# Kernel optimization log

Measured on AMD Instinct MI355X. Metric: run time of the kernel, lower is better.

The kernel has to match this reference:

```python
import jax, jax.numpy as jnp
import numpy as np

B, S, D, H, L, V, F = 4, 2048, 512, 8, 4, 32000, 512
EPS = 1e-3  # keras BatchNormalization default epsilon


def setup_inputs() -> dict:
    key = jax.random.key(0)
    ks = jax.random.split(key, 32)
    n = lambda k, shp, sc=0.02: (jax.random.normal(k, shp, jnp.float32) * sc)
    inp = {
        "sequence": jax.random.randint(ks[0], (B, S), 0, V, dtype=jnp.int32),
        # padding mask: 1 for kept tokens, 0 for padded; broadcast over [B,h,S,S]
        "padding_mask": (jax.random.uniform(ks[1], (B, 1, 1, S)) > 0.1).astype(jnp.float32),
        "pos_embeddings": n(ks[2], (S, D), 1.0),
        "emb": n(ks[3], (V, D), 1.0),
        "wq": n(ks[4], (L, D, D)), "bq": jnp.zeros((L, D), jnp.float32),
        "wk": n(ks[5], (L, D, D)), "bk": jnp.zeros((L, D), jnp.float32),
        "wv": n(ks[6], (L, D, D)), "bv": jnp.zeros((L, D), jnp.float32),
        "wo": n(ks[7], (L, D, D)), "bo": jnp.zeros((L, D), jnp.float32),
        "an_gamma": 1.0 + n(ks[8], (L, D)), "an_beta": n(ks[9], (L, D)),
        "an_mean": n(ks[10], (L, D), 0.1), "an_var": 0.5 + jax.random.uniform(ks[11], (L, D)),
        "d1_w": n(ks[12], (L, D, F)), "d1_b": jnp.zeros((L, F), jnp.float32),
        "d2_w": n(ks[13], (L, F, D)), "d2_b": jnp.zeros((L, D), jnp.float32),
        "fn_gamma": 1.0 + n(ks[14], (L, D)), "fn_beta": n(ks[15], (L, D)),
        "fn_mean": n(ks[16], (L, D), 0.1), "fn_var": 0.5 + jax.random.uniform(ks[17], (L, D)),
    }
    return inp


def _bn(x, gamma, beta, mean, var):
    # keras BatchNormalization in inference mode (moving statistics), axis=-1
    return (x - mean) * jax.lax.rsqrt(var + EPS) * gamma + beta


def reference(sequence, padding_mask, pos_embeddings, emb,
              wq, bq, wk, bk, wv, bv, wo, bo,
              an_gamma, an_beta, an_mean, an_var,
              d1_w, d1_b, d2_w, d2_b,
              fn_gamma, fn_beta, fn_mean, fn_var):
    b, s = sequence.shape
    nlayers, d, _ = wq.shape
    h = H
    dk = d // h
    scale = 1.0 / jnp.sqrt(jnp.float32(dk))

    x = emb[sequence] + pos_embeddings[:s, :]  # [B,S,D]

    def split_heads(t):  # [B,S,D] -> [B,h,S,dk]
        return t.reshape(b, s, h, dk).transpose(0, 2, 1, 3)

    for i in range(nlayers):
        q = split_heads(x @ wq[i] + bq[i])
        k = split_heads(x @ wk[i] + bk[i])
        v = split_heads(x @ wv[i] + bv[i])
        score = jnp.einsum('bhqd,bhkd->bhqk', q, k) * scale  # [B,h,S,S]
        if padding_mask is not None:
            score = score * padding_mask
            score = jnp.where(score == 0, jnp.float32(-1e9), score)
        align = jax.nn.softmax(score, axis=-1)
        ctx = jnp.einsum('bhqk,bhkd->bhqd', align, v)
        ctx = ctx.transpose(0, 2, 1, 3).reshape(b, s, d)
        heads = ctx @ wo[i] + bo[i]
        sub = _bn(x + heads, an_gamma[i], an_beta[i], an_mean[i], an_var[i])
        ffn = jax.nn.relu(sub @ d1_w[i] + d1_b[i]) @ d2_w[i] + d2_b[i]
        x = _bn(sub + ffn, fn_gamma[i], fn_beta[i], fn_mean[i], fn_var[i])
    return x
```

## Files before the change

kernel.cpp:

```cpp
#include <hip/hip_runtime.h>
#include <stdint.h>
#include <stddef.h>

constexpr int BB = 4, SS = 2048, DD = 512, HH = 8, LL = 4;
constexpr int NTOK = BB * SS;
constexpr float BN_EPS = 1e-3f;

using bh = __bf16;
typedef __bf16 bf16x8 __attribute__((ext_vector_type(8)));
typedef float  f32x4  __attribute__((ext_vector_type(4)));

#define DEV __device__ __forceinline__
#define WAITVM(n) asm volatile("s_waitcnt vmcnt(" #n ")" ::: "memory")
#define WAITLGKM0 asm volatile("s_waitcnt lgkmcnt(0)" ::: "memory")

DEV void gload_lds16(const void* g, void* l) {
    __builtin_amdgcn_global_load_lds(
        (const __attribute__((address_space(1))) void*)g,
        (__attribute__((address_space(3))) void*)l, 16, 0, 0);
}

__global__ void wprep(const float* __restrict__ in, bh* __restrict__ out, int ostride) {
    __shared__ float t[32][33];
    const float* ip = in + (size_t)blockIdx.z * DD * DD;
    bh* op = out + (size_t)blockIdx.z * ostride;
    const int r0 = blockIdx.y * 32, c0 = blockIdx.x * 32;
    const int tx = threadIdx.x, ty = threadIdx.y;
    #pragma unroll
    for (int i = ty; i < 32; i += 8) t[i][tx] = ip[(size_t)(r0 + i) * DD + c0 + tx];
    __syncthreads();
    #pragma unroll
    for (int i = ty; i < 32; i += 8) op[(size_t)(c0 + i) * DD + r0 + tx] = (bh)t[tx][i];
}

__global__ void maskprep(const float* __restrict__ mask, float* __restrict__ mb) {
    const int i = ((int)blockIdx.x * 256 + threadIdx.x) * 4;
    const float4 m4 = *(const float4*)(mask + i);
    float4 o;
    o.x = (m4.x == 0.f) ? -1e30f : 0.f;
    o.y = (m4.y == 0.f) ? -1e30f : 0.f;
    o.z = (m4.z == 0.f) ? -1e30f : 0.f;
    o.w = (m4.w == 0.f) ? -1e30f : 0.f;
    *(float4*)(mb + i) = o;
}

__global__ void embed_k(const int* __restrict__ seq, const float* __restrict__ emb,
                        const float* __restrict__ pos, bh* __restrict__ xb) {
    const int m = blockIdx.x;
    const int s = m & (SS - 1);
    const int tok = seq[m];
    const int d = threadIdx.x * 4;
    const float4 e  = *(const float4*)(emb + (size_t)tok * DD + d);
    const float4 pz = *(const float4*)(pos + (size_t)s * DD + d);
    union { bh h[4]; uint64_t u; } pk;
    pk.h[0] = (bh)(e.x + pz.x); pk.h[1] = (bh)(e.y + pz.y);
    pk.h[2] = (bh)(e.z + pz.z); pk.h[3] = (bh)(e.w + pz.w);
    *(uint64_t*)(xb + (size_t)m * DD + d) = pk.u;
}


template <int EP, bool WF32>
__global__ __launch_bounds__(256, 2)
void gemm_bt(const bh* __restrict__ A, const bh* __restrict__ Bt,
             const float* __restrict__ bias, bh* __restrict__ outb,
             const bh* __restrict__ resb, float* __restrict__ Xo,
             const float* __restrict__ gamma, const float* __restrict__ beta,
             const float* __restrict__ mean, const float* __restrict__ var) {
    constexpr int BM = 128, BN = 64, BK = 64, NKT = DD / BK;
    __shared__ __align__(16) bh As[2][BM * BK];
    __shared__ __align__(16) bh Bs[2][BN * BK];

    const int tid = threadIdx.x;
    const int w = tid >> 6, lane = tid & 63;
    const int l15 = lane & 15, l4 = lane >> 4;
    const int i = (int)blockIdx.x;
    const int xcd = i & 7, j = i >> 3;
    const int bm = xcd * 8 + (j >> 3);
    const int bn = j & 7;
    const int m0 = bm * BM, n0 = bn * BN;
    const int wr = w >> 1, wc = w & 1;

    f32x4 acc[4][2] = {};
    const int sr = lane >> 3;
    const int cbx = (lane & 7) ^ sr;

    auto stage = [&](int buf, int kk) {
        #pragma unroll
        for (int ii = 0; ii < 4; ++ii) {
            const int idx = w * 4 + ii;
            const int r = idx * 8 + sr;
            gload_lds16(A + (size_t)(m0 + r) * DD + kk + 8 * cbx, &As[buf][idx * 512]);
        }
        #pragma unroll
        for (int ii = 0; ii < 2; ++ii) {
            const int idx = w * 2 + ii;
            const int r = idx * 8 + sr;
            gload_lds16(Bt + (size_t)(n0 + r) * DD + kk + 8 * cbx, &Bs[buf][idx * 512]);
        }
    };

    stage(0, 0);
    stage(1, BK);

    for (int kt = 0; kt < NKT; ++kt) {
        const int buf = kt & 1;
        if (kt + 1 < NKT) { WAITVM(6); } else { WAITVM(0); }
        __builtin_amdgcn_s_barrier();

        const char* Ab = (const char*)&As[buf][0];
        const char* Bb = (const char*)&Bs[buf][0];
        #pragma unroll
        for (int ks = 0; ks < 2; ++ks) {
            bf16x8 af[4], bfr[2];
            const int cby = ks * 64 + l4 * 16;
            #pragma unroll
            for (int mf = 0; mf < 4; ++mf) {
                const int row = wr * 64 + mf * 16 + l15;
                af[mf] = *(const bf16x8*)(Ab + row * 128 + (cby ^ ((row & 7) << 4)));
            }
            #pragma unroll
            for (int nf = 0; nf < 2; ++nf) {
                const int row = wc * 32 + nf * 16 + l15;
                bfr[nf] = *(const bf16x8*)(Bb + row * 128 + (cby ^ ((row & 7) << 4)));
            }
            #pragma unroll
            for (int mf = 0; mf < 4; ++mf)
                #pragma unroll
                for (int nf = 0; nf < 2; ++nf)
                    acc[mf][nf] = __builtin_amdgcn_mfma_f32_16x16x32_bf16(
                        af[mf], bfr[nf], acc[mf][nf], 0, 0, 0);
        }
        WAITLGKM0;
        __builtin_amdgcn_s_barrier();
        if (kt + 2 < NKT) stage(buf, (kt + 2) * BK);
    }

    #pragma unroll
    for (int nf = 0; nf < 2; ++nf) {
        const int n = n0 + wc * 32 + nf * 16 + l15;
        const float bi = bias[n];
        float g = 0.f, be = 0.f, mu = 0.f, iv = 0.f;
        if constexpr (EP == 1) {
            g = gamma[n]; be = beta[n]; mu = mean[n];
            iv = rsqrtf(var[n] + BN_EPS);
        }
        #pragma unroll
        for (int mf = 0; mf < 4; ++mf) {
            #pragma unroll
            for (int r = 0; r < 4; ++r) {
                const int m = m0 + wr * 64 + mf * 16 + l4 * 4 + r;
                const size_t off = (size_t)m * DD + n;
                const float v = acc[mf][nf][r] + bi;
                if constexpr (EP == 2) {
                    outb[off] = (bh)fmaxf(v, 0.f);
                } else {
                    const float t = (float)resb[off] + v;
                    const float s = (t - mu) * iv * g + be;
                    outb[off] = (bh)s;
                    if constexpr (WF32) Xo[off] = s;
                }
            }
        }
    }
}

__global__ __launch_bounds__(256, 3)
void gemm_qkv(const bh* __restrict__ A, const bh* __restrict__ Bt,
              const float* __restrict__ bq, const float* __restrict__ bk,
              const float* __restrict__ bv,
              bh* __restrict__ qb, bh* __restrict__ kb, bh* __restrict__ vT) {
    constexpr int BM = 128, BN = 64, BK = 64, NKT = DD / BK;
    __shared__ __align__(16) bh As[2][BM * BK];
    __shared__ __align__(16) bh Bs[2][BN * BK];

    const int tid = threadIdx.x;
    const int w = tid >> 6, lane = tid & 63;
    const int l15 = lane & 15, l4 = lane >> 4;
    const int i = (int)blockIdx.x;
    const int xcd = i & 7, j = i >> 3;
    const int bm = xcd * 8 + (j & 7);
    const int bn = j >> 3;
    const int m0 = bm * BM, n0 = bn * BN;
    const int wr = w >> 1, wc = w & 1;

    f32x4 acc[4][2] = {};
    const int sr = lane >> 3;
    const int cbx = (lane & 7) ^ sr;

    auto stage = [&](int buf, int kk) {
        #pragma unroll
        for (int ii = 0; ii < 4; ++ii) {
            const int idx = w * 4 + ii;
            const int r = idx * 8 + sr;
            gload_lds16(A + (size_t)(m0 + r) * DD + kk + 8 * cbx, &As[buf][idx * 512]);
        }
        #pragma unroll
        for (int ii = 0; ii < 2; ++ii) {
            const int idx = w * 2 + ii;
            const int r = idx * 8 + sr;
            gload_lds16(Bt + (size_t)(n0 + r) * DD + kk + 8 * cbx, &Bs[buf][idx * 512]);
        }
    };

    stage(0, 0);
    stage(1, BK);

    for (int kt = 0; kt < NKT; ++kt) {
        const int buf = kt & 1;
        if (kt + 1 < NKT) { WAITVM(6); } else { WAITVM(0); }
        __builtin_amdgcn_s_barrier();

        const char* Ab = (const char*)&As[buf][0];
        const char* Bb = (const char*)&Bs[buf][0];
        #pragma unroll
        for (int ks = 0; ks < 2; ++ks) {
            bf16x8 af[4], bfr[2];
            const int cby = ks * 64 + l4 * 16;
            #pragma unroll
            for (int mf = 0; mf < 4; ++mf) {
                const int row = wr * 64 + mf * 16 + l15;
                af[mf] = *(const bf16x8*)(Ab + row * 128 + (cby ^ ((row & 7) << 4)));
            }
            #pragma unroll
            for (int nf = 0; nf < 2; ++nf) {
                const int row = wc * 32 + nf * 16 + l15;
                bfr[nf] = *(const bf16x8*)(Bb + row * 128 + (cby ^ ((row & 7) << 4)));
            }
            #pragma unroll
            for (int mf = 0; mf < 4; ++mf)
                #pragma unroll
                for (int nf = 0; nf < 2; ++nf)
                    acc[mf][nf] = __builtin_amdgcn_mfma_f32_16x16x32_bf16(
                        af[mf], bfr[nf], acc[mf][nf], 0, 0, 0);
        }
        WAITLGKM0;
        __builtin_amdgcn_s_barrier();
        if (kt + 2 < NKT) stage(buf, (kt + 2) * BK);
    }

    const int part = n0 >> 9;
    #pragma unroll
    for (int nf = 0; nf < 2; ++nf) {
        const int n = n0 + wc * 32 + nf * 16 + l15;
        const int nn = n & 511;
        const float bi = (part == 0 ? bq : part == 1 ? bk : bv)[nn];
        if (part < 2) {
            bh* out = part ? kb : qb;
            #pragma unroll
            for (int mf = 0; mf < 4; ++mf)
                #pragma unroll
                for (int r = 0; r < 4; ++r) {
                    const int m = m0 + wr * 64 + mf * 16 + l4 * 4 + r;
                    out[(size_t)m * DD + nn] = (bh)(acc[mf][nf][r] + bi);
                }
        } else {
            const int hh = nn >> 6, dk = nn & 63;
            #pragma unroll
            for (int mf = 0; mf < 4; ++mf) {
                const int m = m0 + wr * 64 + mf * 16 + l4 * 4;
                const int bb2 = m >> 11, s = m & (SS - 1);
                union { bh h4[4]; uint64_t u; } pk;
                #pragma unroll
                for (int r = 0; r < 4; ++r)
                    pk.h4[r] = (bh)(acc[mf][nf][r] + bi);
                *(uint64_t*)(vT + ((size_t)((bb2 * HH + hh) * 64) + dk) * SS + s) = pk.u;
            }
        }
    }
}

__global__ __launch_bounds__(128, 2)
void flash_attn(const bh* __restrict__ Q, const bh* __restrict__ K,
                const bh* __restrict__ VT, const float* __restrict__ mb,
                bh* __restrict__ O) {
    constexpr int KVB = 64, NT = SS / KVB;
    constexpr float CSC = 0.18033688f;
    __shared__ __align__(16) bh Ks[2][KVB * 64];
    __shared__ __align__(16) bh Vs[2][64 * KVB];
    __shared__ __align__(16) bh Plds[2][2][16 * 64];

    const int tid = threadIdx.x;
    const int w = tid >> 6, lane = tid & 63;
    const int l15 = lane & 15, l4 = lane >> 4;

    const int i = (int)blockIdx.x;
    const int xcd = i & 7, j = i >> 3;
    const int g = xcd * 4 + (j >> 5);
    const int qt = j & 31;
    const int h = g & 7, b = g >> 3;

    const int q0 = qt * 64 + w * 32;

    bf16x8 qf[2][2];
    #pragma unroll
    for (int st = 0; st < 2; ++st) {
        const bh* qp = Q + (size_t)(b * SS + q0 + st * 16 + l15) * DD + h * 64 + l4 * 8;
        qf[st][0] = *(const bf16x8*)qp;
        qf[st][1] = *(const bf16x8*)(qp + 32);
    }

    f32x4 ctx[2][4] = {};
    f32x4 accl[2] = {};
    float m2[2] = {-3e38f, -3e38f};

    bf16x8 ones;
    #pragma unroll
    for (int z = 0; z < 8; ++z) ones[z] = (bh)1.0f;

    const int sr = lane >> 3;
    const int cbx = (lane & 7) ^ sr;
    const bh* kg = K + (size_t)b * SS * DD + h * 64 + 8 * cbx;
    const bh* vg = VT + (size_t)((b * HH + h) * 64) * SS + 8 * cbx;
    const float* mbb = mb + (size_t)b * SS;

    auto stage = [&](int buf, int kt) {
        #pragma unroll
        for (int ii = 0; ii < 4; ++ii) {
            const int idx = w * 4 + ii;
            const int r = idx * 8 + sr;
            gload_lds16(kg + (size_t)(kt + r) * DD, &Ks[buf][idx * 512]);
        }
        #pragma unroll
        for (int ii = 0; ii < 4; ++ii) {
            const int idx = w * 4 + ii;
            const int r = idx * 8 + sr;
            gload_lds16(vg + (size_t)r * SS + kt, &Vs[buf][idx * 512]);
        }
    };

    f32x4 mbc[4];
    stage(0, 0);
    stage(1, KVB);
    #pragma unroll
    for (int nf = 0; nf < 4; ++nf)
        mbc[nf] = *(const f32x4*)(mbb + nf * 16 + l4 * 4);
    __syncthreads();

    for (int t = 0; t < NT; ++t) {
        const int buf = t & 1;
        const int kt = t * KVB;
        if (t > 0) {
            if (t + 1 < NT) { WAITVM(12); } else { WAITVM(4); }
            __builtin_amdgcn_s_barrier();
        }

        f32x4 sc[2][4] = {};
        const char* Kb = (const char*)&Ks[buf][0];
        #pragma unroll
        for (int ks = 0; ks < 2; ++ks) {
            bf16x8 kf[4];
            #pragma unroll
            for (int nf = 0; nf < 4; ++nf) {
                const int row = nf * 16 + l15;
                kf[nf] = *(const bf16x8*)(Kb + row * 128 +
                          ((ks * 64 + l4 * 16) ^ ((row & 7) << 4)));
            }
            __builtin_amdgcn_s_setprio(1);
            #pragma unroll
            for (int st = 0; st < 2; ++st)
                #pragma unroll
                for (int nf = 0; nf < 4; ++nf)
                    sc[st][nf] = __builtin_amdgcn_mfma_f32_16x16x32_bf16(
                        kf[nf], qf[st][ks], sc[st][nf], 0, 0, 0);
            __builtin_amdgcn_s_setprio(0);
        }

        #pragma unroll
        for (int st = 0; st < 2; ++st) {
            #pragma unroll
            for (int nf = 0; nf < 4; ++nf)
                #pragma unroll
                for (int r = 0; r < 4; ++r)
                    sc[st][nf][r] = fmaf(sc[st][nf][r], CSC, mbc[nf][r]);
            float tm;
            {
                f32x4 m01, m23;
                #pragma unroll
                for (int r = 0; r < 4; ++r) {
                    m01[r] = fmaxf(sc[st][0][r], sc[st][1][r]);
                    m23[r] = fmaxf(sc[st][2][r], sc[st][3][r]);
                }
                const float a = fmaxf(fmaxf(m01[0], m01[1]), fmaxf(m01[2], m01[3]));
                const float c = fmaxf(fmaxf(m23[0], m23[1]), fmaxf(m23[2], m23[3]));
                tm = fmaxf(a, c);
            }
            tm = fmaxf(tm, __shfl_xor(tm, 16, 64));
            tm = fmaxf(tm, __shfl_xor(tm, 32, 64));
            if (__any(tm > m2[st] + 11.5f)) {
                const float mn = fmaxf(fmaxf(tm, m2[st]), -60.f);
                const float fac = __builtin_amdgcn_exp2f(m2[st] - mn);
                m2[st] = mn;
                accl[st] *= fac;
                #pragma unroll
                for (int nf = 0; nf < 4; ++nf)
                    #pragma unroll
                    for (int r = 0; r < 4; ++r)
                        ctx[st][nf][r] *= fac;
            }
            #pragma unroll
            for (int nf = 0; nf < 4; ++nf) {
                union { bh h4[4]; uint64_t u; } pk;
                #pragma unroll
                for (int r = 0; r < 4; ++r)
                    pk.h4[r] = (bh)__builtin_amdgcn_exp2f(sc[st][nf][r] - m2[st]);
                *(uint64_t*)((char*)&Plds[w][st][0] + l15 * 128 +
                             ((nf * 32 + l4 * 8) ^ ((l15 & 7) << 4))) = pk.u;
            }
        }

        const char* Vb = (const char*)&Vs[buf][0];
        #pragma unroll
        for (int ks = 0; ks < 2; ++ks) {
            bf16x8 vf[4];
            #pragma unroll
            for (int nf = 0; nf < 4; ++nf) {
                const int row = nf * 16 + l15;
                vf[nf] = *(const bf16x8*)(Vb + row * 128 +
                          ((ks * 64 + l4 * 16) ^ ((row & 7) << 4)));
            }
            bf16x8 pa[2];
            #pragma unroll
            for (int st = 0; st < 2; ++st)
                pa[st] = *(const bf16x8*)((const char*)&Plds[w][st][0] + l15 * 128 +
                          ((ks * 64 + l4 * 16) ^ ((l15 & 7) << 4)));
            __builtin_amdgcn_s_setprio(1);
            #pragma unroll
            for (int st = 0; st < 2; ++st) {
                #pragma unroll
                for (int nf = 0; nf < 4; ++nf)
                    ctx[st][nf] = __builtin_amdgcn_mfma_f32_16x16x32_bf16(
                        vf[nf], pa[st], ctx[st][nf], 0, 0, 0);
                accl[st] = __builtin_amdgcn_mfma_f32_16x16x32_bf16(
                    ones, pa[st], accl[st], 0, 0, 0);
            }
            __builtin_amdgcn_s_setprio(0);
        }

        WAITLGKM0;
        __builtin_amdgcn_s_barrier();
        if (t + 1 < NT) {
            #pragma unroll
            for (int nf = 0; nf < 4; ++nf)
                mbc[nf] = *(const f32x4*)(mbb + kt + KVB + nf * 16 + l4 * 4);
        }
        if (t + 2 < NT) stage(buf, kt + 2 * KVB);
    }

    #pragma unroll
    for (int st = 0; st < 2; ++st) {
        const float linv = 1.0f / accl[st][0];
        #pragma unroll
        for (int nf = 0; nf < 4; ++nf) {
            union { bh h4[4]; uint64_t u; } pk;
            #pragma unroll
            for (int r = 0; r < 4; ++r)
                pk.h4[r] = (bh)(ctx[st][nf][r] * linv);
            *(uint64_t*)(O + (size_t)(b * SS + q0 + st * 16 + l15) * DD +
                         h * 64 + nf * 16 + l4 * 4) = pk.u;
        }
    }
}

extern "C" void kernel_launch(void* const* d_in, const int* in_sizes, int n_in,
                              void* d_out, int out_size, void* d_ws, size_t ws_size,
                              hipStream_t stream) {
    const int*   seq  = (const int*)  d_in[0];
    const float* mask = (const float*)d_in[1];
    const float* pos  = (const float*)d_in[2];
    const float* emb  = (const float*)d_in[3];
    const float* wq = (const float*)d_in[4];  const float* bq = (const float*)d_in[5];
    const float* wk = (const float*)d_in[6];  const float* bk = (const float*)d_in[7];
    const float* wv = (const float*)d_in[8];  const float* bv = (const float*)d_in[9];
    const float* wo = (const float*)d_in[10]; const float* bo = (const float*)d_in[11];
    const float* ag = (const float*)d_in[12]; const float* ab = (const float*)d_in[13];
    const float* am = (const float*)d_in[14]; const float* av = (const float*)d_in[15];
    const float* d1w = (const float*)d_in[16]; const float* d1b = (const float*)d_in[17];
    const float* d2w = (const float*)d_in[18]; const float* d2b = (const float*)d_in[19];
    const float* fg = (const float*)d_in[20]; const float* fb = (const float*)d_in[21];
    const float* fm = (const float*)d_in[22]; const float* fv = (const float*)d_in[23];

    float* X = (float*)d_out;

    char* p = (char*)d_ws;
    auto take = [&](size_t n) { char* q = p; p += (n + 255) & ~(size_t)255; return q; };
    const size_t WE  = (size_t)LL * DD * DD;
    const size_t WQE = (size_t)LL * 3 * DD * DD;
    bh* wcat = (bh*)take(WQE * 2);
    bh* wot = (bh*)take(WE * 2);
    bh* w1t = (bh*)take(WE * 2);
    bh* w2t = (bh*)take(WE * 2);
    const size_t AE = (size_t)NTOK * DD;
    bh* xb   = (bh*)take(AE * 2);
    bh* qb   = (bh*)take(AE * 2);
    bh* kb   = (bh*)take(AE * 2);
    bh* ctxb = (bh*)take(AE * 2);
    bh* subb = (bh*)take(AE * 2);
    bh* h1b  = (bh*)take(AE * 2);
    bh* vT   = (bh*)take(AE * 2);
    float* mbias = (float*)take((size_t)BB * SS * 4);

    const int QKV_OS = 3 * DD * DD;
    const dim3 wg(16, 16, LL), wb(32, 8);
    wprep<<<wg, wb, 0, stream>>>(wq,  wcat + 0 * DD * DD, QKV_OS);
    wprep<<<wg, wb, 0, stream>>>(wk,  wcat + 1 * DD * DD, QKV_OS);
    wprep<<<wg, wb, 0, stream>>>(wv,  wcat + 2 * DD * DD, QKV_OS);
    wprep<<<wg, wb, 0, stream>>>(wo,  wot, DD * DD);
    wprep<<<wg, wb, 0, stream>>>(d1w, w1t, DD * DD);
    wprep<<<wg, wb, 0, stream>>>(d2w, w2t, DD * DD);

    maskprep<<<dim3(BB * SS / 1024), dim3(256), 0, stream>>>(mask, mbias);
    embed_k<<<dim3(NTOK), dim3(128), 0, stream>>>(seq, emb, pos, xb);

    for (int l = 0; l < LL; ++l) {
        const size_t wof = (size_t)l * DD * DD;
        const int    bof = l * DD;
        gemm_qkv<<<dim3(1536), dim3(256), 0, stream>>>(
            xb, wcat + (size_t)l * QKV_OS, bq + bof, bk + bof, bv + bof, qb, kb, vT);
        flash_attn<<<dim3(1024), dim3(128), 0, stream>>>(qb, kb, vT, mbias, ctxb);
        gemm_bt<1, false><<<dim3(512), dim3(256), 0, stream>>>(
            ctxb, wot + wof, bo + bof, subb, xb, nullptr,
            ag + bof, ab + bof, am + bof, av + bof);
        gemm_bt<2, false><<<dim3(512), dim3(256), 0, stream>>>(
            subb, w1t + wof, d1b + bof, h1b, nullptr, nullptr,
            nullptr, nullptr, nullptr, nullptr);
        if (l + 1 < LL) {
            gemm_bt<1, false><<<dim3(512), dim3(256), 0, stream>>>(
                h1b, w2t + wof, d2b + bof, xb, subb, nullptr,
                fg + bof, fb + bof, fm + bof, fv + bof);
        } else {
            gemm_bt<1, true><<<dim3(512), dim3(256), 0, stream>>>(
                h1b, w2t + wof, d2b + bof, xb, subb, X,
                fg + bof, fb + bof, fm + bof, fv + bof);
        }
    }
}
```

Before: 480.6 us.

## Shrink GEMM and attention tiles, restructure attention to one q-tile per wave

The dense GEMMs switch from 128x64 to 64x64 tiles with twice as many blocks and a higher occupancy target. Their double-buffer schedule now prefetches the next K slice before computing the current one, and the MFMA section runs at raised priority. Flash attention now uses 4 waves of 16 query rows each and a KV block of 32, with a padded P scratch buffer and a new V swizzle. The aim is better occupancy and latency hiding, at the cost of less data reuse per block and more loop iterations and barriers.

```diff
diff --git a/kernel.cpp b/kernel.cpp
--- a/kernel.cpp
+++ b/kernel.cpp
@@ -58,64 +58,58 @@
     *(uint64_t*)(xb + (size_t)m * DD + d) = pk.u;
 }
 
-
 template <int EP, bool WF32>
-__global__ __launch_bounds__(256, 2)
-void gemm_bt(const bh* __restrict__ A, const bh* __restrict__ Bt,
-             const float* __restrict__ bias, bh* __restrict__ outb,
-             const bh* __restrict__ resb, float* __restrict__ Xo,
-             const float* __restrict__ gamma, const float* __restrict__ beta,
-             const float* __restrict__ mean, const float* __restrict__ var) {
-    constexpr int BM = 128, BN = 64, BK = 64, NKT = DD / BK;
-    __shared__ __align__(16) bh As[2][BM * BK];
-    __shared__ __align__(16) bh Bs[2][BN * BK];
+__global__ __launch_bounds__(256, 4)
+void gemm64(const bh* __restrict__ A, const bh* __restrict__ Bt,
+            const float* __restrict__ bias, bh* __restrict__ outb,
+            const bh* __restrict__ resb, float* __restrict__ Xo,
+            const float* __restrict__ gamma, const float* __restrict__ beta,
+            const float* __restrict__ mean, const float* __restrict__ var) {
+    constexpr int BK = 64, NKT = DD / BK;
+    __shared__ __align__(16) bh As[2][64 * BK];
+    __shared__ __align__(16) bh Bs[2][64 * BK];
 
     const int tid = threadIdx.x;
     const int w = tid >> 6, lane = tid & 63;
     const int l15 = lane & 15, l4 = lane >> 4;
     const int i = (int)blockIdx.x;
     const int xcd = i & 7, j = i >> 3;
-    const int bm = xcd * 8 + (j >> 3);
+    const int bm = xcd * 16 + (j >> 3);
     const int bn = j & 7;
-    const int m0 = bm * BM, n0 = bn * BN;
+    const int m0 = bm * 64, n0 = bn * 64;
     const int wr = w >> 1, wc = w & 1;
 
-    f32x4 acc[4][2] = {};
+    f32x4 acc[2][2] = {};
     const int sr = lane >> 3;
     const int cbx = (lane & 7) ^ sr;
 
     auto stage = [&](int buf, int kk) {
-        #pragma unroll
-        for (int ii = 0; ii < 4; ++ii) {
-            const int idx = w * 4 + ii;
-            const int r = idx * 8 + sr;
-            gload_lds16(A + (size_t)(m0 + r) * DD + kk + 8 * cbx, &As[buf][idx * 512]);
-        }
         #pragma unroll
         for (int ii = 0; ii < 2; ++ii) {
             const int idx = w * 2 + ii;
             const int r = idx * 8 + sr;
+            gload_lds16(A + (size_t)(m0 + r) * DD + kk + 8 * cbx, &As[buf][idx * 512]);
             gload_lds16(Bt + (size_t)(n0 + r) * DD + kk + 8 * cbx, &Bs[buf][idx * 512]);
         }
     };
 
     stage(0, 0);
-    stage(1, BK);
+    __syncthreads();
 
     for (int kt = 0; kt < NKT; ++kt) {
         const int buf = kt & 1;
-        if (kt + 1 < NKT) { WAITVM(6); } else { WAITVM(0); }
-        __builtin_amdgcn_s_barrier();
+        if (kt > 0) { WAITVM(0); __builtin_amdgcn_s_barrier(); }
+        if (kt + 1 < NKT) stage(buf ^ 1, (kt + 1) * BK);
 
         const char* Ab = (const char*)&As[buf][0];
         const char* Bb = (const char*)&Bs[buf][0];
         #pragma unroll
         for (int ks = 0; ks < 2; ++ks) {
-            bf16x8 af[4], bfr[2];
+            bf16x8 af[2], bfr[2];
             const int cby = ks * 64 + l4 * 16;
             #pragma unroll
-            for (int mf = 0; mf < 4; ++mf) {
-                const int row = wr * 64 + mf * 16 + l15;
+            for (int mf = 0; mf < 2; ++mf) {
+                const int row = wr * 32 + mf * 16 + l15;
                 af[mf] = *(const bf16x8*)(Ab + row * 128 + (cby ^ ((row & 7) << 4)));
             }
             #pragma unroll
@@ -123,16 +117,15 @@
                 const int row = wc * 32 + nf * 16 + l15;
                 bfr[nf] = *(const bf16x8*)(Bb + row * 128 + (cby ^ ((row & 7) << 4)));
             }
-            #pragma unroll
-            for (int mf = 0; mf < 4; ++mf)
+            __builtin_amdgcn_s_setprio(1);
+            #pragma unroll
+            for (int mf = 0; mf < 2; ++mf)
                 #pragma unroll
                 for (int nf = 0; nf < 2; ++nf)
                     acc[mf][nf] = __builtin_amdgcn_mfma_f32_16x16x32_bf16(
                         af[mf], bfr[nf], acc[mf][nf], 0, 0, 0);
-        }
-        WAITLGKM0;
-        __builtin_amdgcn_s_barrier();
-        if (kt + 2 < NKT) stage(buf, (kt + 2) * BK);
+            __builtin_amdgcn_s_setprio(0);
+        }
     }
 
     #pragma unroll
@@ -145,10 +138,10 @@
             iv = rsqrtf(var[n] + BN_EPS);
         }
         #pragma unroll
-        for (int mf = 0; mf < 4; ++mf) {
+        for (int mf = 0; mf < 2; ++mf) {
             #pragma unroll
             for (int r = 0; r < 4; ++r) {
-                const int m = m0 + wr * 64 + mf * 16 + l4 * 4 + r;
+                const int m = m0 + wr * 32 + mf * 16 + l4 * 4 + r;
                 const size_t off = (size_t)m * DD + n;
                 const float v = acc[mf][nf][r] + bi;
                 if constexpr (EP == 2) {
@@ -269,15 +262,15 @@
     }
 }
 
-__global__ __launch_bounds__(128, 2)
+__global__ __launch_bounds__(256, 4)
 void flash_attn(const bh* __restrict__ Q, const bh* __restrict__ K,
                 const bh* __restrict__ VT, const float* __restrict__ mb,
                 bh* __restrict__ O) {
-    constexpr int KVB = 64, NT = SS / KVB;
+    constexpr int KVB = 32, NT = SS / KVB;
     constexpr float CSC = 0.18033688f;
     __shared__ __align__(16) bh Ks[2][KVB * 64];
     __shared__ __align__(16) bh Vs[2][64 * KVB];
-    __shared__ __align__(16) bh Plds[2][2][16 * 64];
+    __shared__ __align__(16) bh Plds[4][16 * 40];
 
     const int tid = threadIdx.x;
     const int w = tid >> 6, lane = tid & 63;
@@ -289,175 +282,130 @@
     const int qt = j & 31;
     const int h = g & 7, b = g >> 3;
 
-    const int q0 = qt * 64 + w * 32;
-
-    bf16x8 qf[2][2];
-    #pragma unroll
-    for (int st = 0; st < 2; ++st) {
-        const bh* qp = Q + (size_t)(b * SS + q0 + st * 16 + l15) * DD + h * 64 + l4 * 8;
-        qf[st][0] = *(const bf16x8*)qp;
-        qf[st][1] = *(const bf16x8*)(qp + 32);
-    }
-
-    f32x4 ctx[2][4] = {};
-    f32x4 accl[2] = {};
-    float m2[2] = {-3e38f, -3e38f};
+    const int q0 = qt * 64 + w * 16;
+
+    const bh* qp = Q + (size_t)(b * SS + q0 + l15) * DD + h * 64 + l4 * 8;
+    const bf16x8 qf0 = *(const bf16x8*)qp;
+    const bf16x8 qf1 = *(const bf16x8*)(qp + 32);
+
+    f32x4 ctx[4] = {};
+    f32x4 accl = {};
+    float m2 = -3e38f;
 
     bf16x8 ones;
     #pragma unroll
     for (int z = 0; z < 8; ++z) ones[z] = (bh)1.0f;
 
-    const int sr = lane >> 3;
-    const int cbx = (lane & 7) ^ sr;
-    const bh* kg = K + (size_t)b * SS * DD + h * 64 + 8 * cbx;
-    const bh* vg = VT + (size_t)((b * HH + h) * 64) * SS + 8 * cbx;
-    const float* mbb = mb + (size_t)b * SS;
+    const int ksr = lane >> 3;
+    const int kcb = (lane & 7) ^ ksr;
+    const int vrow = lane >> 2;
+    const int vcb  = (lane & 3) ^ (vrow & 3);
+
+    const bh* kg = K + ((size_t)(b * SS) + w * 8 + ksr) * DD + h * 64 + 8 * kcb;
+    const bh* vg = VT + ((size_t)((b * HH + h) * 64) + w * 16 + vrow) * SS + 8 * vcb;
+    const float* mbb = mb + (size_t)b * SS + l4 * 4;
 
     auto stage = [&](int buf, int kt) {
-        #pragma unroll
-        for (int ii = 0; ii < 4; ++ii) {
-            const int idx = w * 4 + ii;
-            const int r = idx * 8 + sr;
-            gload_lds16(kg + (size_t)(kt + r) * DD, &Ks[buf][idx * 512]);
-        }
-        #pragma unroll
-        for (int ii = 0; ii < 4; ++ii) {
-            const int idx = w * 4 + ii;
-            const int r = idx * 8 + sr;
-            gload_lds16(vg + (size_t)r * SS + kt, &Vs[buf][idx * 512]);
-        }
+        gload_lds16(kg + (size_t)kt * DD, &Ks[buf][w * 512]);
+        gload_lds16(vg + kt,              &Vs[buf][w * 512]);
     };
 
-    f32x4 mbc[4];
+    f32x4 mbc[2];
     stage(0, 0);
-    stage(1, KVB);
-    #pragma unroll
-    for (int nf = 0; nf < 4; ++nf)
-        mbc[nf] = *(const f32x4*)(mbb + nf * 16 + l4 * 4);
+    mbc[0] = *(const f32x4*)(mbb);
+    mbc[1] = *(const f32x4*)(mbb + 16);
     __syncthreads();
 
     for (int t = 0; t < NT; ++t) {
         const int buf = t & 1;
         const int kt = t * KVB;
-        if (t > 0) {
-            if (t + 1 < NT) { WAITVM(12); } else { WAITVM(4); }
-            __builtin_amdgcn_s_barrier();
-        }
-
-        f32x4 sc[2][4] = {};
+        if (t > 0) { WAITVM(2); __builtin_amdgcn_s_barrier(); }
+        if (t + 1 < NT) stage(buf ^ 1, kt + KVB);
+
         const char* Kb = (const char*)&Ks[buf][0];
-        #pragma unroll
-        for (int ks = 0; ks < 2; ++ks) {
-            bf16x8 kf[4];
-            #pragma unroll
-            for (int nf = 0; nf < 4; ++nf) {
+        bf16x8 kf[2][2];
+        #pragma unroll
+        for (int ks = 0; ks < 2; ++ks)
+            #pragma unroll
+            for (int nf = 0; nf < 2; ++nf) {
                 const int row = nf * 16 + l15;
-                kf[nf] = *(const bf16x8*)(Kb + row * 128 +
-                          ((ks * 64 + l4 * 16) ^ ((row & 7) << 4)));
-            }
-            __builtin_amdgcn_s_setprio(1);
-            #pragma unroll
-            for (int st = 0; st < 2; ++st)
-                #pragma unroll
-                for (int nf = 0; nf < 4; ++nf)
-                    sc[st][nf] = __builtin_amdgcn_mfma_f32_16x16x32_bf16(
-                        kf[nf], qf[st][ks], sc[st][nf], 0, 0, 0);
-            __builtin_amdgcn_s_setprio(0);
-        }
-
-        #pragma unroll
-        for (int st = 0; st < 2; ++st) {
+                kf[ks][nf] = *(const bf16x8*)(Kb + row * 128 +
+                              ((ks * 64 + l4 * 16) ^ ((row & 7) << 4)));
+            }
+        f32x4 sc[2] = {};
+        __builtin_amdgcn_s_setprio(1);
+        #pragma unroll
+        for (int ks = 0; ks < 2; ++ks)
+            #pragma unroll
+            for (int nf = 0; nf < 2; ++nf)
+                sc[nf] = __builtin_amdgcn_mfma_f32_16x16x32_bf16(
+                    kf[ks][nf], ks ? qf1 : qf0, sc[nf], 0, 0, 0);
+        __builtin_amdgcn_s_setprio(0);
+
+        float tm = -3e38f;
+        #pragma unroll
+        for (int nf = 0; nf < 2; ++nf)
+            #pragma unroll
+            for (int r = 0; r < 4; ++r) {
+                const float z = fmaf(sc[nf][r], CSC, mbc[nf][r]);
+                sc[nf][r] = z;
+                tm = fmaxf(tm, z);
+            }
+        if (__any(tm > m2 + 11.5f)) {
+            tm = fmaxf(tm, __shfl_xor(tm, 16, 64));
+            tm = fmaxf(tm, __shfl_xor(tm, 32, 64));
+            const float mn = fmaxf(fmaxf(tm, m2), -60.f);
+            const float fac = __builtin_amdgcn_exp2f(m2 - mn);
+            m2 = mn;
+            accl *= fac;
             #pragma unroll
             for (int nf = 0; nf < 4; ++nf)
                 #pragma unroll
                 for (int r = 0; r < 4; ++r)
-                    sc[st][nf][r] = fmaf(sc[st][nf][r], CSC, mbc[nf][r]);
-            float tm;
-            {
-                f32x4 m01, m23;
-                #pragma unroll
-                for (int r = 0; r < 4; ++r) {
-                    m01[r] = fmaxf(sc[st][0][r], sc[st][1][r]);
-                    m23[r] = fmaxf(sc[st][2][r], sc[st][3][r]);
-                }
-                const float a = fmaxf(fmaxf(m01[0], m01[1]), fmaxf(m01[2], m01[3]));
-                const float c = fmaxf(fmaxf(m23[0], m23[1]), fmaxf(m23[2], m23[3]));
-                tm = fmaxf(a, c);
-            }
-            tm = fmaxf(tm, __shfl_xor(tm, 16, 64));
-            tm = fmaxf(tm, __shfl_xor(tm, 32, 64));
-            if (__any(tm > m2[st] + 11.5f)) {
-                const float mn = fmaxf(fmaxf(tm, m2[st]), -60.f);
-                const float fac = __builtin_amdgcn_exp2f(m2[st] - mn);
-                m2[st] = mn;
-                accl[st] *= fac;
-                #pragma unroll
-                for (int nf = 0; nf < 4; ++nf)
-                    #pragma unroll
-                    for (int r = 0; r < 4; ++r)
-                        ctx[st][nf][r] *= fac;
-            }
-            #pragma unroll
-            for (int nf = 0; nf < 4; ++nf) {
-                union { bh h4[4]; uint64_t u; } pk;
-                #pragma unroll
-                for (int r = 0; r < 4; ++r)
-                    pk.h4[r] = (bh)__builtin_amdgcn_exp2f(sc[st][nf][r] - m2[st]);
-                *(uint64_t*)((char*)&Plds[w][st][0] + l15 * 128 +
-                             ((nf * 32 + l4 * 8) ^ ((l15 & 7) << 4))) = pk.u;
-            }
-        }
+                    ctx[nf][r] *= fac;
+        }
+
+        char* Pw = (char*)&Plds[w][0] + l15 * 80;
+        #pragma unroll
+        for (int nf = 0; nf < 2; ++nf) {
+            union { bh h4[4]; uint64_t u; } pk;
+            #pragma unroll
+            for (int r = 0; r < 4; ++r)
+                pk.h4[r] = (bh)__builtin_amdgcn_exp2f(sc[nf][r] - m2);
+            *(uint64_t*)(Pw + nf * 32 + l4 * 8) = pk.u;
+        }
+        WAITLGKM0;
+        const bf16x8 pa = *(const bf16x8*)(Pw + l4 * 16);
 
         const char* Vb = (const char*)&Vs[buf][0];
-        #pragma unroll
-        for (int ks = 0; ks < 2; ++ks) {
-            bf16x8 vf[4];
-            #pragma unroll
-            for (int nf = 0; nf < 4; ++nf) {
-                const int row = nf * 16 + l15;
-                vf[nf] = *(const bf16x8*)(Vb + row * 128 +
-                          ((ks * 64 + l4 * 16) ^ ((row & 7) << 4)));
-            }
-            bf16x8 pa[2];
-            #pragma unroll
-            for (int st = 0; st < 2; ++st)
-                pa[st] = *(const bf16x8*)((const char*)&Plds[w][st][0] + l15 * 128 +
-                          ((ks * 64 + l4 * 16) ^ ((l15 & 7) << 4)));
-            __builtin_amdgcn_s_setprio(1);
-            #pragma unroll
-            for (int st = 0; st < 2; ++st) {
-                #pragma unroll
-                for (int nf = 0; nf < 4; ++nf)
-                    ctx[st][nf] = __builtin_amdgcn_mfma_f32_16x16x32_bf16(
-                        vf[nf], pa[st], ctx[st][nf], 0, 0, 0);
-                accl[st] = __builtin_amdgcn_mfma_f32_16x16x32_bf16(
-                    ones, pa[st], accl[st], 0, 0, 0);
-            }
-            __builtin_amdgcn_s_setprio(0);
-        }
-
-        WAITLGKM0;
-        __builtin_amdgcn_s_barrier();
+        bf16x8 vf[4];
+        #pragma unroll
+        for (int nf = 0; nf < 4; ++nf) {
+            const int row = nf * 16 + l15;
+            vf[nf] = *(const bf16x8*)(Vb + row * 64 + ((l4 ^ (l15 & 3)) << 4));
+        }
+        __builtin_amdgcn_s_setprio(1);
+        #pragma unroll
+        for (int nf = 0; nf < 4; ++nf)
+            ctx[nf] = __builtin_amdgcn_mfma_f32_16x16x32_bf16(vf[nf], pa, ctx[nf], 0, 0, 0);
+        accl = __builtin_amdgcn_mfma_f32_16x16x32_bf16(ones, pa, accl, 0, 0, 0);
+        __builtin_amdgcn_s_setprio(0);
+
         if (t + 1 < NT) {
-            #pragma unroll
-            for (int nf = 0; nf < 4; ++nf)
-                mbc[nf] = *(const f32x4*)(mbb + kt + KVB + nf * 16 + l4 * 4);
-        }
-        if (t + 2 < NT) stage(buf, kt + 2 * KVB);
-    }
-
-    #pragma unroll
-    for (int st = 0; st < 2; ++st) {
-        const float linv = 1.0f / accl[st][0];
-        #pragma unroll
-        for (int nf = 0; nf < 4; ++nf) {
-            union { bh h4[4]; uint64_t u; } pk;
-            #pragma unroll
-            for (int r = 0; r < 4; ++r)
-                pk.h4[r] = (bh)(ctx[st][nf][r] * linv);
-            *(uint64_t*)(O + (size_t)(b * SS + q0 + st * 16 + l15) * DD +
-                         h * 64 + nf * 16 + l4 * 4) = pk.u;
-        }
+            mbc[0] = *(const f32x4*)(mbb + kt + KVB);
+            mbc[1] = *(const f32x4*)(mbb + kt + KVB + 16);
+        }
+    }
+
+    const float linv = 1.0f / accl[0];
+    #pragma unroll
+    for (int nf = 0; nf < 4; ++nf) {
+        union { bh h4[4]; uint64_t u; } pk;
+        #pragma unroll
+        for (int r = 0; r < 4; ++r)
+            pk.h4[r] = (bh)(ctx[nf][r] * linv);
+        *(uint64_t*)(O + (size_t)(b * SS + q0 + l15) * DD +
+                     h * 64 + nf * 16 + l4 * 4) = pk.u;
     }
 }
 
@@ -516,19 +464,19 @@
         const int    bof = l * DD;
         gemm_qkv<<<dim3(1536), dim3(256), 0, stream>>>(
             xb, wcat + (size_t)l * QKV_OS, bq + bof, bk + bof, bv + bof, qb, kb, vT);
-        flash_attn<<<dim3(1024), dim3(128), 0, stream>>>(qb, kb, vT, mbias, ctxb);
-        gemm_bt<1, false><<<dim3(512), dim3(256), 0, stream>>>(
+        flash_attn<<<dim3(1024), dim3(256), 0, stream>>>(qb, kb, vT, mbias, ctxb);
+        gemm64<1, false><<<dim3(1024), dim3(256), 0, stream>>>(
             ctxb, wot + wof, bo + bof, subb, xb, nullptr,
             ag + bof, ab + bof, am + bof, av + bof);
-        gemm_bt<2, false><<<dim3(512), dim3(256), 0, stream>>>(
+        gemm64<2, false><<<dim3(1024), dim3(256), 0, stream>>>(
             subb, w1t + wof, d1b + bof, h1b, nullptr, nullptr,
             nullptr, nullptr, nullptr, nullptr);
         if (l + 1 < LL) {
-            gemm_bt<1, false><<<dim3(512), dim3(256), 0, stream>>>(
+            gemm64<1, false><<<dim3(1024), dim3(256), 0, stream>>>(
                 h1b, w2t + wof, d2b + bof, xb, subb, nullptr,
                 fg + bof, fb + bof, fm + bof, fv + bof);
         } else {
-            gemm_bt<1, true><<<dim3(512), dim3(256), 0, stream>>>(
+            gemm64<1, true><<<dim3(1024), dim3(256), 0, stream>>>(
                 h1b, w2t + wof, d2b + bof, xb, subb, X,
                 fg + bof, fb + bof, fm + bof, fv + bof);
         }
```

Measured after the change: 467.9 us. -2.6%, faster.
